# Performance work log

Measured on AMD Instinct MI355X. Metric: run time of the kernel, lower is better.

Reference implementation:

```python
import jax, jax.numpy as jnp
import numpy as np

_SQRT1_2 = 0.7071067811865476

B, S, D, N, NCH = 4, 2048, 1024, 32768, 8


def setup_inputs() -> dict:
    key = jax.random.key(0)
    ks = jax.random.split(key, 6)
    return {
        "x": jax.random.normal(ks[0], (B, S, D), jnp.float32),
        "h": jax.random.normal(ks[1], (B, S, D), jnp.float32),
        "emb": jax.random.normal(ks[2], (N, D), jnp.float32),
        "tau_offset": jax.random.normal(ks[3], (B, S, 1), jnp.float32),
        "w_read": jax.random.normal(ks[4], (N, D), jnp.float32),
        "w_write": jax.random.normal(ks[5], (N, D), jnp.float32),
        "n_chunks": NCH,
    }


def _srw_chunked(x, h, emb_unit, tau_offset, w_read, w_write, n_chunks):
    b, s, d = x.shape
    n = emb_unit.shape[0]
    cs = n // n_chunks
    h_bf = h.astype(jnp.bfloat16)
    x_bf = x.astype(jnp.bfloat16)
    emb_bf = emb_unit.astype(jnp.bfloat16)
    read_bf = w_read.astype(jnp.bfloat16)
    write_bf = w_write.astype(jnp.bfloat16)
    z1 = jnp.zeros((b, s, 1), jnp.float32)

    # ---- pass 1: online score statistics over chunks of N ----
    @jax.checkpoint
    def stats_step(carry, i):
        s_sum, sq_sum, cube_sum, ns_sum, ns_sq = carry
        ec = jax.lax.dynamic_slice_in_dim(emb_bf, i * cs, cs, axis=0)
        sc = (h_bf @ ec.T).astype(jnp.float32)  # [B,S,cs]
        s_sum = s_sum + sc.sum(-1, keepdims=True)
        sq_sum = sq_sum + (sc ** 2).sum(-1, keepdims=True)
        cube_sum = cube_sum + (sc ** 3).sum(-1, keepdims=True)
        pns = sc.mean(axis=(0, 1))  # per-neuron mean score [cs]
        return ((s_sum, sq_sum, cube_sum, ns_sum + pns.sum(), ns_sq + (pns ** 2).sum()), None)

    (s_sum, sq_sum, cube_sum, ns_sum, ns_sq), _ = jax.lax.scan(
        stats_step, (z1, z1, z1, jnp.float32(0.0), jnp.float32(0.0)), jnp.arange(n_chunks))

    s_mean = s_sum / n
    s_std = jnp.sqrt(sq_sum / n - s_mean ** 2) + 1e-08
    tau = s_mean + tau_offset * s_std
    cube_mean = cube_sum / n
    central_third = cube_mean - 3.0 * s_mean * s_std ** 2 - s_mean ** 3
    score_skew = jax.lax.stop_gradient((central_third / (s_std ** 3 + 1e-08)).mean())
    mean_score = ns_sum / n
    var_score = ns_sq / n - mean_score ** 2
    score_lb = var_score / (mean_score ** 2 + var_score + 0.01)

    # ---- pass 2: erf-threshold gate + read/write GEMM accumulate ----
    @jax.checkpoint
    def gate_step(carry, i):
        out, wcost, gmax, act, strong, phib, zsum, z075c, z030c, glg = carry
        s0 = i * cs
        ec = jax.lax.dynamic_slice_in_dim(emb_bf, s0, cs, axis=0)
        rc = jax.lax.dynamic_slice_in_dim(read_bf, s0, cs, axis=0)
        wc = jax.lax.dynamic_slice_in_dim(write_bf, s0, cs, axis=0)
        rc = rc / (jnp.linalg.norm(rc, axis=-1, keepdims=True) + 1e-08)
        wc = wc / (jnp.linalg.norm(wc, axis=-1, keepdims=True) + 1e-08)
        z = ((h_bf @ ec.T).astype(jnp.float32) - tau) / s_std  # [B,S,cs]
        phi = 0.5 * (1.0 + jax.lax.erf(z * _SQRT1_2))
        gate = jnp.where(z > 0, z * phi, 0.0)
        xr = x_bf @ rc.T  # [B,S,cs]
        c_out = ((gate.astype(jnp.bfloat16) * xr) @ wc).astype(jnp.float32)  # [B,S,D]
        g_safe = gate + 1e-08
        new = (
            out + c_out,
            wcost + gate.sum(-1, keepdims=True),
            jnp.maximum(gmax, gate.max(-1, keepdims=True)),
            act + (gate > 0.0).astype(jnp.float32).sum(-1, keepdims=True),
            strong + (gate > 0.5).astype(jnp.float32).sum(-1, keepdims=True),
            phib + ((phi > 0.95) | (phi < 0.05)).astype(jnp.float32).sum(-1, keepdims=True),
            zsum + jnp.where(z > 0, z, 0.0).sum(-1, keepdims=True),
            z075c + ((z > 0) & (z < 0.75)).astype(jnp.float32).sum(-1, keepdims=True),
            z030c + ((z > 0) & (z < 0.3)).astype(jnp.float32).sum(-1, keepdims=True),
            glg + (gate * jnp.log(g_safe)).sum(-1, keepdims=True),
        )
        return (new, None)

    init = (jnp.zeros((b, s, d), jnp.float32), z1, jnp.full((b, s, 1), -1e9, jnp.float32),
            z1, z1, z1, z1, z1, z1, z1)
    (raw_out, wcost, gmax, act, strong, phib, zsum, z075c, z030c, glg), _ = jax.lax.scan(
        gate_step, init, jnp.arange(n_chunks))

    den = jnp.maximum(wcost, 1.0)
    out = (raw_out / den).astype(jnp.bfloat16)
    score_std_out = s_std.mean()
    es_out = wcost.mean()
    active_n_mean = act.mean()
    z_mean_active = zsum / (act + 1e-08)
    active_eps = act + 1e-08
    z_lt_075_frac = jax.lax.stop_gradient((z075c / active_eps).mean())
    z_lt_030_frac = jax.lax.stop_gradient((z030c / active_eps).mean())
    tau_abs_mean = jax.lax.stop_gradient(tau).mean()
    active_per_token_std = jax.lax.stop_gradient(act).std()
    gate_sum_eps = wcost + 1e-08
    entropy_per_token = -glg / gate_sum_eps + jnp.log(gate_sum_eps)
    gate_entropy = jax.lax.stop_gradient(entropy_per_token).mean()
    return (out.astype(jnp.float32), act / n, gmax, score_lb, score_std_out, es_out,
            active_n_mean, strong / n, phib / n, z_mean_active, tau_abs_mean,
            z_lt_075_frac, z_lt_030_frac, score_skew, active_per_token_std, gate_entropy)


def reference(x, h, emb, tau_offset, w_read, w_write, n_chunks):
    emb_unit = emb / (jnp.linalg.norm(emb, axis=-1, keepdims=True) + 1e-08)
    return _srw_chunked(x, h, emb_unit, tau_offset, w_read, w_write, n_chunks)
```

## Files before the change

kernel.cpp:

```cpp
#include <hip/hip_runtime.h>

#define DEV __device__ __forceinline__

typedef __attribute__((ext_vector_type(4))) float f32x4;
typedef __attribute__((ext_vector_type(8))) short s16x8;
typedef __attribute__((ext_vector_type(8))) unsigned short u16x8;

static const int NTOK = 8192;
static const int DD   = 1024;
static const int NNEU = 32768;
static const int NC   = 8192;
static const int NREP = 8;

static const int OUT_ACT    = 8388608;
static const int OUT_GMAX   = 8396800;
static const int OUT_SLB    = 8404992;
static const int OUT_SSTD   = 8404993;
static const int OUT_ES     = 8404994;
static const int OUT_ANM    = 8404995;
static const int OUT_STRONG = 8404996;
static const int OUT_PHIB   = 8413188;
static const int OUT_ZMEAN  = 8421380;
static const int OUT_TAUM   = 8429572;
static const int OUT_Z75    = 8429573;
static const int OUT_Z30    = 8429574;
static const int OUT_SKEW   = 8429575;
static const int OUT_ASTD   = 8429576;
static const int OUT_ENT    = 8429577;

DEV unsigned short f2bf(float f){
  unsigned u = __float_as_uint(f);
  u += 0x7fffu + ((u >> 16) & 1u);
  return (unsigned short)(u >> 16);
}
DEV float bf2f(unsigned short h){ return __uint_as_float(((unsigned)h) << 16); }
DEV float rnd_bf(float f){ return bf2f(f2bf(f)); }

template<int AUX>
DEV void gl_lds16(const void* g, void* l){
  __builtin_amdgcn_global_load_lds(
      (const __attribute__((address_space(1))) unsigned int*)g,
      (__attribute__((address_space(3))) unsigned int*)l, 16, 0, AUX);
}

DEV f32x4 mfma16(s16x8 a, s16x8 b, f32x4 c){
  return __builtin_amdgcn_mfma_f32_16x16x32_bf16(a, b, c, 0, 0, 0);
}

template<int AUX>
DEV void stage4(const unsigned short* __restrict__ G, size_t ld, int k0,
                unsigned short* L, int t){
  #pragma unroll
  for (int i = 0; i < 4; i++){
    int ch = i*256 + t;
    int row = ch >> 3, c = ch & 7;
    int cs = c ^ (row & 7);
    int wb = (i*256 + (t & 192)) * 16;
    gl_lds16<AUX>(G + (size_t)row * ld + k0 + cs*8, (char*)L + wb);
  }
}

DEV void stageS(const unsigned short* __restrict__ S0, size_t ldS,
                unsigned short* L, int t){
  #pragma unroll
  for (int i = 0; i < 8; i++){
    int ch = i*256 + t;
    int row = ch >> 4, c = ch & 15;
    int cs = c ^ (row & 15);
    int wb = (i*256 + (t & 192)) * 16;
    gl_lds16<0>(S0 + (size_t)row * ldS + cs*8, (char*)L + wb);
  }
}

DEV s16x8 frg(const unsigned short* L, int R, int kk, int lq){
  int cc = ((kk >> 3) + lq) ^ (R & 7);
  return *(const s16x8*)((const char*)L + R*128 + cc*16);
}

DEV void waitv_bar(){
  asm volatile("s_waitcnt vmcnt(0)" ::: "memory");
  __builtin_amdgcn_s_barrier();
  __builtin_amdgcn_sched_barrier(0);
}

DEV int2 xcd64(){
  int orig = blockIdx.y * 64 + blockIdx.x;
  int xcd = orig & 7, p = orig >> 3;
  int sqy = p >> 6, off = p & 63;
  int2 r;
  r.x = xcd*8 + (off & 7);
  r.y = sqy*8 + (off >> 3);
  return r;
}


template<int RND, int PNS>
__global__ __launch_bounds__(256) void k_rncast(const float* __restrict__ in,
    unsigned short* __restrict__ o, const float* __restrict__ hs,
    float* __restrict__ ns){
  __shared__ float hsh[1024];
  __shared__ float pr[8];
  int t = threadIdx.x, l = t & 63, wv = t >> 6;
  if (PNS){
    for (int i = t; i < 1024; i += 256) hsh[i] = hs[i];
    __syncthreads();
  }
  int row = blockIdx.x * 4 + wv;
  const float4* rp = (const float4*)(in + (size_t)row * DD);
  float4 v[4];
  float ss = 0.f;
  #pragma unroll
  for (int j = 0; j < 4; j++){
    float4 a = rp[j*64 + l];
    if (RND){ a.x = rnd_bf(a.x); a.y = rnd_bf(a.y); a.z = rnd_bf(a.z); a.w = rnd_bf(a.w); }
    v[j] = a;
    ss += a.x*a.x + a.y*a.y + a.z*a.z + a.w*a.w;
  }
  #pragma unroll
  for (int d = 1; d < 64; d <<= 1) ss += __shfl_xor(ss, d);
  float inv = 1.f / (sqrtf(ss) + 1e-8f);
  float dot = 0.f;
  ushort4* op = (ushort4*)(o + (size_t)row * DD);
  #pragma unroll
  for (int j = 0; j < 4; j++){
    ushort4 r;
    r.x = f2bf(v[j].x * inv); r.y = f2bf(v[j].y * inv);
    r.z = f2bf(v[j].z * inv); r.w = f2bf(v[j].w * inv);
    op[j*64 + l] = r;
    if (PNS){
      int c0 = (j*64 + l)*4;
      dot += hsh[c0]*bf2f(r.x) + hsh[c0+1]*bf2f(r.y)
           + hsh[c0+2]*bf2f(r.z) + hsh[c0+3]*bf2f(r.w);
    }
  }
  if (PNS){
    #pragma unroll
    for (int d = 1; d < 64; d <<= 1) dot += __shfl_xor(dot, d);
    if (l == 0){
      float pns = dot * (1.f / 8192.f);
      pr[wv*2] = pns; pr[wv*2 + 1] = pns*pns;
    }
    __syncthreads();
    if (t == 0){
      atomicAdd(ns + 0, pr[0] + pr[2] + pr[4] + pr[6]);
      atomicAdd(ns + 1, pr[1] + pr[3] + pr[5] + pr[7]);
    }
  }
}

__global__ __launch_bounds__(256) void k_wnorm(const float* __restrict__ w_,
                                               float* __restrict__ inv_w){
  int t = threadIdx.x, l = t & 63, wv = t >> 6;
  int row = blockIdx.x * 4 + wv;
  const float4* wp = (const float4*)(w_ + (size_t)row * DD);
  float sw = 0.f;
  #pragma unroll
  for (int j = 0; j < 4; j++){
    float4 c = wp[j*64 + l];
    float c0 = rnd_bf(c.x), c1 = rnd_bf(c.y), c2 = rnd_bf(c.z), c3 = rnd_bf(c.w);
    sw += c0*c0 + c1*c1 + c2*c2 + c3*c3;
  }
  #pragma unroll
  for (int d = 1; d < 64; d <<= 1) sw += __shfl_xor(sw, d);
  if (l == 0) inv_w[row] = 1.f / (sqrtf(sw) + 1e-8f);
}

__global__ __launch_bounds__(256) void k_cast(const float* __restrict__ in,
                                              unsigned short* __restrict__ o){
  size_t i = (size_t)blockIdx.x * 256 + threadIdx.x;
  float4 v = ((const float4*)in)[i];
  ushort4 r;
  r.x = f2bf(v.x); r.y = f2bf(v.y); r.z = f2bf(v.z); r.w = f2bf(v.w);
  ((ushort4*)o)[i] = r;
}

__global__ __launch_bounds__(256) void k_wcnT(const float* __restrict__ w_,
    const float* __restrict__ invw, unsigned short* __restrict__ o){
  __shared__ unsigned short tile[64][65];
  int t = threadIdx.x;
  int n0b = blockIdx.x * 64, d0 = blockIdx.y * 64;
  #pragma unroll
  for (int i = 0; i < 16; i++){
    int idx = t + i*256;
    int r = idx >> 6, c = idx & 63;
    float v = w_[(size_t)(n0b + r) * DD + d0 + c];
    tile[c][r] = f2bf(rnd_bf(v) * invw[n0b + r]);
  }
  __syncthreads();
  #pragma unroll
  for (int i = 0; i < 16; i++){
    int idx = t + i*256;
    int rd = idx >> 6, cn = idx & 63;
    o[(size_t)(d0 + rd) * NNEU + n0b + cn] = tile[rd][cn];
  }
}

__global__ __launch_bounds__(256) void k_hsum(const unsigned short* __restrict__ hb,
                                              float* __restrict__ hs){
  int t = threadIdx.x; int r0 = blockIdx.x * 128;
  float s[4] = {0.f, 0.f, 0.f, 0.f};
  for (int r = 0; r < 128; r++){
    const unsigned short* row = hb + (size_t)(r0 + r) * DD;
    #pragma unroll
    for (int j = 0; j < 4; j++) s[j] += bf2f(row[j*256 + t]);
  }
  #pragma unroll
  for (int j = 0; j < 4; j++) atomicAdd(hs + j*256 + t, s[j]);
}


template<bool DO_STATS>
__global__ __launch_bounds__(256, 2) void k_score(
    const unsigned short* __restrict__ A, const unsigned short* __restrict__ Bm,
    float* __restrict__ s_sum, float* __restrict__ sq_sum, float* __restrict__ cu_sum,
    unsigned short* __restrict__ Sout, int do_store)
{
  __shared__ unsigned short lds[32768];
  const int t = threadIdx.x, l = t & 63, wv = t >> 6;
  const int wm = wv >> 1, wn = wv & 1;
  const int lq = l >> 4, lr = l & 15;
  int2 rm = xcd64();
  const int bx = rm.x, by = rm.y;
  const unsigned short* Ab = A  + (size_t)by * 128 * DD;
  const unsigned short* Bb = Bm + (size_t)bx * 128 * DD;
  f32x4 acc[4][4];
  #pragma unroll
  for (int m = 0; m < 4; m++)
    #pragma unroll
    for (int n = 0; n < 4; n++) acc[m][n] = (f32x4){0.f, 0.f, 0.f, 0.f};

  stage4<0>(Ab, DD, 0, lds, t);
  stage4<0>(Bb, DD, 0, lds + 8192, t);
  waitv_bar();
  int cur = 0;
  for (int ks = 0; ks < 16; ++ks){
    unsigned short* Lc = lds + cur*16384;
    if (ks + 1 < 16){
      unsigned short* Ln = lds + (cur^1)*16384;
      int k0 = (ks+1)*64;
      stage4<0>(Ab, DD, k0, Ln, t);
      stage4<0>(Bb, DD, k0, Ln + 8192, t);
    }
    #pragma unroll
    for (int kk = 0; kk < 64; kk += 32){
      s16x8 af[4], bf4[4];
      #pragma unroll
      for (int m = 0; m < 4; m++) af[m]  = frg(Lc, wm*64 + m*16 + lr, kk, lq);
      #pragma unroll
      for (int n = 0; n < 4; n++) bf4[n] = frg(Lc + 8192, wn*64 + n*16 + lr, kk, lq);
      #pragma unroll
      for (int m = 0; m < 4; m++)
        #pragma unroll
        for (int n = 0; n < 4; n++)
          acc[m][n] = mfma16(af[m], bf4[n], acc[m][n]);
    }
    waitv_bar();
    cur ^= 1;
  }

  unsigned short* sl = lds;
  #pragma unroll
  for (int m = 0; m < 4; m++)
  #pragma unroll
  for (int n = 0; n < 4; n++)
  #pragma unroll
  for (int r = 0; r < 4; r++){
    int rl = wm*64 + m*16 + lq*4 + r;
    int cl = wn*64 + n*16 + lr;
    sl[rl*136 + cl] = f2bf(acc[m][n][r]);
  }
  __syncthreads();

  int row = t >> 1, half = t & 1;
  const unsigned short* sp = &sl[row*136 + half*64];
  unsigned short* Sdst = Sout + (size_t)(by*128 + row) * NC + bx*128 + half*64;
  float s1 = 0.f, s2 = 0.f, s3 = 0.f;
  #pragma unroll
  for (int j = 0; j < 8; j++){
    u16x8 v = *(const u16x8*)(sp + j*8);
    if (do_store) *(u16x8*)(Sdst + j*8) = v;
    if (DO_STATS){
      #pragma unroll
      for (int e = 0; e < 8; e++){
        float f = bf2f(v[e]);
        s1 += f; float f2 = f*f; s2 += f2; s3 += f2*f;
      }
    }
  }
  if (DO_STATS){
    s1 += __shfl_xor(s1, 1); s2 += __shfl_xor(s2, 1); s3 += __shfl_xor(s3, 1);
    if (half == 0){
      int gr = by*128 + row;
      int rep = (bx & 7) * NTOK;
      atomicAdd(s_sum + rep + gr, s1);
      atomicAdd(sq_sum + rep + gr, s2);
      atomicAdd(cu_sum + rep + gr, s3);
    }
  }
}

__global__ __launch_bounds__(256) void k_tau(const float* __restrict__ s_sum,
    const float* __restrict__ sq_sum, const float* __restrict__ tof,
    float* __restrict__ tau, float* __restrict__ rstd){
  int i = blockIdx.x * 256 + threadIdx.x;
  float ssum = 0.f, sqsum = 0.f;
  #pragma unroll
  for (int k = 0; k < NREP; k++){
    ssum  += s_sum[k*NTOK + i];
    sqsum += sq_sum[k*NTOK + i];
  }
  float mean = ssum * (1.f / 32768.f);
  float var  = sqsum * (1.f / 32768.f) - mean*mean;
  float sstd = sqrtf(fmaxf(var, 0.f)) + 1e-8f;
  tau[i]  = mean + tof[i] * sstd;
  rstd[i] = 1.f / sstd;
}

DEV void gate_epilogue(unsigned short* lds, unsigned short* SP,
    const float* tau, const float* rstd, int bx, int by, int t,
    float* wcostp, float* gmaxp, float* actp, float* strongp, float* phibp,
    float* zsump, float* z075p, float* z030p, float* glgp)
{
  int row = t >> 1, half = t & 1;
  int gr = by*128 + row;
  float tauv = tau[gr], rs = rstd[gr];
  unsigned short* Prow = SP + (size_t)gr * NC + bx*128 + half*64;
  float wsum = 0.f, gmx = 0.f, ac = 0.f, stc = 0.f, pb = 0.f;
  float zs = 0.f, z7 = 0.f, z3 = 0.f, gl = 0.f;
  #pragma unroll
  for (int jj = 0; jj < 8; jj++){
    int g  = half*8 + jj;
    int cs = g ^ (row & 15);
    u16x8 s8 = *(const u16x8*)&lds[row*128 + cs*8];
    u16x8 x8 = *(const u16x8*)&lds[16384 + row*128 + cs*8];
    u16x8 pv;
    #pragma unroll
    for (int e = 0; e < 8; e++){
      float sc = bf2f(s8[e]);
      float xr = bf2f(x8[e]);
      float z = (sc - tauv) * rs;
      float phi = 0.5f * (1.0f + erff(z * 0.70710678118654752440f));
      float gate = (z > 0.f) ? z * phi : 0.f;
      wsum += gate; gmx = fmaxf(gmx, gate);
      if (gate > 0.5f) stc += 1.f;
      if (fabsf(z) > 1.6448536f) pb += 1.f;
      if (z > 0.f){ ac += 1.f; zs += z; if (z < 0.75f) z7 += 1.f; if (z < 0.3f) z3 += 1.f; }
      gl += gate * __logf(gate + 1e-8f);
      pv[e] = f2bf(rnd_bf(gate) * xr);
    }
    *(u16x8*)(Prow + jj*8) = pv;
  }
  wsum += __shfl_xor(wsum, 1); gmx = fmaxf(gmx, __shfl_xor(gmx, 1));
  ac   += __shfl_xor(ac, 1);   stc += __shfl_xor(stc, 1);
  pb   += __shfl_xor(pb, 1);   zs  += __shfl_xor(zs, 1);
  z7   += __shfl_xor(z7, 1);   z3  += __shfl_xor(z3, 1);
  gl   += __shfl_xor(gl, 1);
  if (half == 0){
    int rep = (bx & 7) * NTOK;
    atomicAdd(wcostp + rep + gr, wsum);
    atomicMax((int*)(gmaxp + rep + gr), __float_as_int(gmx));
    atomicAdd(actp + rep + gr, ac);
    atomicAdd(strongp + rep + gr, stc);
    atomicAdd(phibp + rep + gr, pb);
    atomicAdd(zsump + rep + gr, zs);
    atomicAdd(z075p + rep + gr, z7);
    atomicAdd(z030p + rep + gr, z3);
    atomicAdd(glgp + rep + gr, gl);
  }
}


__global__ __launch_bounds__(256, 2) void k_gateS(
    const unsigned short* __restrict__ Xb, const unsigned short* __restrict__ Rb,
    const float* __restrict__ tau, const float* __restrict__ rstd,
    unsigned short* __restrict__ SP, int n0,
    float* __restrict__ wcostp, float* __restrict__ gmaxp, float* __restrict__ actp,
    float* __restrict__ strongp, float* __restrict__ phibp, float* __restrict__ zsump,
    float* __restrict__ z075p, float* __restrict__ z030p, float* __restrict__ glgp)
{
  __shared__ unsigned short lds[32768];
  const int t = threadIdx.x, l = t & 63, wv = t >> 6;
  const int wm = wv >> 1, wn = wv & 1;
  const int lq = l >> 4, lr = l & 15;
  int2 rm = xcd64();
  const int bx = rm.x, by = rm.y;
  const unsigned short* Xp = Xb + (size_t)by * 128 * DD;
  const unsigned short* Rp = Rb + (size_t)(n0 + bx*128) * DD;
  const unsigned short* Stile = SP + (size_t)(by*128) * NC + bx*128;
  f32x4 accX[4][4];
  #pragma unroll
  for (int m = 0; m < 4; m++)
    #pragma unroll
    for (int n = 0; n < 4; n++) accX[m][n] = (f32x4){0.f,0.f,0.f,0.f};

  stage4<0>(Xp, DD, 0, lds, t);
  stage4<0>(Rp, DD, 0, lds + 8192, t);
  waitv_bar();
  int cur = 0;
  for (int ks = 0; ks < 16; ++ks){
    unsigned short* Lc = lds + cur*16384;
    if (ks + 1 < 16){
      unsigned short* Ln = lds + (cur^1)*16384;
      int k0 = (ks+1)*64;
      stage4<0>(Xp, DD, k0, Ln, t);
      stage4<0>(Rp, DD, k0, Ln + 8192, t);
    } else {
      stageS(Stile, NC, lds, t);
    }
    #pragma unroll
    for (int kk = 0; kk < 64; kk += 32){
      s16x8 af[4], bf4[4];
      #pragma unroll
      for (int m = 0; m < 4; m++) af[m]  = frg(Lc, wm*64 + m*16 + lr, kk, lq);
      #pragma unroll
      for (int n = 0; n < 4; n++) bf4[n] = frg(Lc + 8192, wn*64 + n*16 + lr, kk, lq);
      #pragma unroll
      for (int m = 0; m < 4; m++)
        #pragma unroll
        for (int n = 0; n < 4; n++)
          accX[m][n] = mfma16(af[m], bf4[n], accX[m][n]);
    }
    waitv_bar();
    cur ^= 1;
  }
  unsigned short* xrl = lds + 16384;
  #pragma unroll
  for (int m = 0; m < 4; m++)
  #pragma unroll
  for (int n = 0; n < 4; n++)
  #pragma unroll
  for (int r = 0; r < 4; r++){
    int rl = wm*64 + m*16 + lq*4 + r;
    int cl = wn*64 + n*16 + lr;
    int cs = (cl >> 3) ^ (rl & 15);
    xrl[rl*128 + cs*8 + (cl & 7)] = f2bf(accX[m][n][r]);
  }
  __syncthreads();

  gate_epilogue(lds, SP, tau, rstd, bx, by, t,
      wcostp, gmaxp, actp, strongp, phibp, zsump, z075p, z030p, glgp);
}


__global__ __launch_bounds__(256, 2) void k_gate_dual(
    const unsigned short* __restrict__ Hb, const unsigned short* __restrict__ Ec,
    const unsigned short* __restrict__ Xb, const unsigned short* __restrict__ Rc,
    const float* __restrict__ tau, const float* __restrict__ rstd,
    unsigned short* __restrict__ SP,
    float* __restrict__ wcostp, float* __restrict__ gmaxp, float* __restrict__ actp,
    float* __restrict__ strongp, float* __restrict__ phibp, float* __restrict__ zsump,
    float* __restrict__ z075p, float* __restrict__ z030p, float* __restrict__ glgp)
{
  __shared__ unsigned short lds[32768];
  const int t = threadIdx.x, l = t & 63, wv = t >> 6;
  const int wm = wv >> 1, wn = wv & 1;
  const int lq = l >> 4, lr = l & 15;
  int2 rm = xcd64();
  const int bx = rm.x, by = rm.y;
  const unsigned short* Hp = Hb + (size_t)by * 128 * DD;
  const unsigned short* Xp = Xb + (size_t)by * 128 * DD;
  const unsigned short* Ep = Ec + (size_t)(bx*128) * DD;
  const unsigned short* Rp = Rc + (size_t)(bx*128) * DD;
  f32x4 accS[4][4], accX[4][4];
  #pragma unroll
  for (int m = 0; m < 4; m++)
    #pragma unroll
    for (int n = 0; n < 4; n++){
      accS[m][n] = (f32x4){0.f,0.f,0.f,0.f};
      accX[m][n] = (f32x4){0.f,0.f,0.f,0.f};
    }

  for (int k0 = 0; k0 < DD; k0 += 64){
    __syncthreads();
    stage4<0>(Hp, DD, k0, lds +     0, t);
    stage4<0>(Ep, DD, k0, lds +  8192, t);
    stage4<0>(Xp, DD, k0, lds + 16384, t);
    stage4<0>(Rp, DD, k0, lds + 24576, t);
    asm volatile("s_waitcnt vmcnt(0)" ::: "memory");
    __syncthreads();
    #pragma unroll
    for (int kk = 0; kk < 64; kk += 32){
      s16x8 af[4], bf4[4];
      #pragma unroll
      for (int m = 0; m < 4; m++) af[m]  = frg(lds, wm*64 + m*16 + lr, kk, lq);
      #pragma unroll
      for (int n = 0; n < 4; n++) bf4[n] = frg(lds + 8192, wn*64 + n*16 + lr, kk, lq);
      #pragma unroll
      for (int m = 0; m < 4; m++)
        #pragma unroll
        for (int n = 0; n < 4; n++)
          accS[m][n] = mfma16(af[m], bf4[n], accS[m][n]);
      #pragma unroll
      for (int m = 0; m < 4; m++) af[m]  = frg(lds + 16384, wm*64 + m*16 + lr, kk, lq);
      #pragma unroll
      for (int n = 0; n < 4; n++) bf4[n] = frg(lds + 24576, wn*64 + n*16 + lr, kk, lq);
      #pragma unroll
      for (int m = 0; m < 4; m++)
        #pragma unroll
        for (int n = 0; n < 4; n++)
          accX[m][n] = mfma16(af[m], bf4[n], accX[m][n]);
    }
  }
  __syncthreads();
  #pragma unroll
  for (int m = 0; m < 4; m++)
  #pragma unroll
  for (int n = 0; n < 4; n++)
  #pragma unroll
  for (int r = 0; r < 4; r++){
    int rl = wm*64 + m*16 + lq*4 + r;
    int cl = wn*64 + n*16 + lr;
    int cs = (cl >> 3) ^ (rl & 15);
    lds[rl*128 + cs*8 + (cl & 7)]         = f2bf(accS[m][n][r]);
    lds[16384 + rl*128 + cs*8 + (cl & 7)] = f2bf(accX[m][n][r]);
  }
  __syncthreads();

  gate_epilogue(lds, SP, tau, rstd, bx, by, t,
      wcostp, gmaxp, actp, strongp, phibp, zsump, z075p, z030p, glgp);
}

__global__ __launch_bounds__(256) void k_redw(const float* __restrict__ wcostp,
                                              float* __restrict__ wc){
  int i = blockIdx.x * 256 + threadIdx.x;
  float s = 0.f;
  #pragma unroll
  for (int k = 0; k < NREP; k++) s += wcostp[k*NTOK + i];
  wc[i] = s;
}


__global__ __launch_bounds__(256, 2) void k_out_gemm(
    const unsigned short* __restrict__ Pm, const unsigned short* __restrict__ Bt,
    float* __restrict__ outp, const float* __restrict__ wcost, int accum, int fin)
{
  __shared__ unsigned short lds[32768];
  const int t = threadIdx.x, l = t & 63, wv = t >> 6;
  const int wm = wv >> 1, wn = wv & 1;
  const int lq = l >> 4, lr = l & 15;
  const int bx = blockIdx.x, by = blockIdx.y;
  const unsigned short* Ab = Pm + (size_t)by * 128 * NC;
  const unsigned short* Bb = Bt + (size_t)bx * 128 * NNEU;
  f32x4 acc[4][4];
  #pragma unroll
  for (int m = 0; m < 4; m++)
    #pragma unroll
    for (int n = 0; n < 4; n++) acc[m][n] = (f32x4){0.f,0.f,0.f,0.f};

  const int NT = NC / 64;
  stage4<2>(Ab, NC, 0, lds, t);
  stage4<0>(Bb, NNEU, 0, lds + 8192, t);
  waitv_bar();
  int cur = 0;
  for (int ks = 0; ks < NT; ++ks){
    unsigned short* Lc = lds + cur*16384;
    if (ks + 1 < NT){
      unsigned short* Ln = lds + (cur^1)*16384;
      int k0 = (ks+1)*64;
      stage4<2>(Ab, NC, k0, Ln, t);
      stage4<0>(Bb, NNEU, k0, Ln + 8192, t);
    }
    #pragma unroll
    for (int kk = 0; kk < 64; kk += 32){
      s16x8 af[4], bf4[4];
      #pragma unroll
      for (int m = 0; m < 4; m++) af[m]  = frg(Lc, wm*64 + m*16 + lr, kk, lq);
      #pragma unroll
      for (int n = 0; n < 4; n++) bf4[n] = frg(Lc + 8192, wn*64 + n*16 + lr, kk, lq);
      #pragma unroll
      for (int m = 0; m < 4; m++)
        #pragma unroll
        for (int n = 0; n < 4; n++)
          acc[m][n] = mfma16(af[m], bf4[n], acc[m][n]);
    }
    waitv_bar();
    cur ^= 1;
  }
  #pragma unroll
  for (int m = 0; m < 4; m++)
  #pragma unroll
  for (int r = 0; r < 4; r++){
    int gr = by*128 + wm*64 + m*16 + lq*4 + r;
    float den = fin ? fmaxf(wcost[gr], 1.f) : 1.f;
    #pragma unroll
    for (int n = 0; n < 4; n++){
      int dc = bx*128 + wn*64 + n*16 + lr;
      float* o = outp + (size_t)gr * DD + dc;
      float v = acc[m][n][r];
      if (accum) v += *o;
      if (fin)   v = rnd_bf(v / den);
      *o = v;
    }
  }
}


__global__ __launch_bounds__(1024) void k_final(
    const float* __restrict__ s_sum, const float* __restrict__ sq_sum,
    const float* __restrict__ cu_sum, const float* __restrict__ tof,
    const float* __restrict__ wcostp, const float* __restrict__ gmaxp,
    const float* __restrict__ actp, const float* __restrict__ strongp,
    const float* __restrict__ phibp, const float* __restrict__ zsump,
    const float* __restrict__ z075p, const float* __restrict__ z030p,
    const float* __restrict__ glgp, const float* __restrict__ ns,
    float* __restrict__ out)
{
  int tid = threadIdx.x;
  float s0=0,s1=0,s2=0,s3=0,s4=0,s5=0,s6=0,s7=0,s8=0;
  for (int i = tid; i < NTOK; i += 1024){
    float ssum=0, sqsum=0, cusum=0, wc=0, gmax=0, ac=0, stc=0, pb=0, zsv=0, z7=0, z3=0, glv=0;
    #pragma unroll
    for (int k = 0; k < NREP; k++){
      int o = k*NTOK + i;
      ssum += s_sum[o]; sqsum += sq_sum[o]; cusum += cu_sum[o];
      wc += wcostp[o]; gmax = fmaxf(gmax, gmaxp[o]);
      ac += actp[o]; stc += strongp[o]; pb += phibp[o];
      zsv += zsump[o]; z7 += z075p[o]; z3 += z030p[o]; glv += glgp[o];
    }
    float mean = ssum * (1.f / 32768.f);
    float var  = sqsum * (1.f / 32768.f) - mean*mean;
    float sstd = sqrtf(fmaxf(var, 0.f)) + 1e-8f;
    float tauv = mean + tof[i] * sstd;
    out[OUT_ACT + i]    = ac * (1.f / 32768.f);
    out[OUT_GMAX + i]   = gmax;
    out[OUT_STRONG + i] = stc * (1.f / 32768.f);
    out[OUT_PHIB + i]   = pb * (1.f / 32768.f);
    out[OUT_ZMEAN + i]  = zsv / (ac + 1e-8f);
    float c3 = cusum * (1.f / 32768.f) - 3.f*mean*sstd*sstd - mean*mean*mean;
    float skew = c3 / (sstd*sstd*sstd + 1e-8f);
    float gse = wc + 1e-8f;
    float ent = -glv / gse + logf(gse);
    s0 += sstd; s1 += wc; s2 += ac; s3 += ac*ac; s4 += tauv;
    s5 += z7 / (ac + 1e-8f); s6 += z3 / (ac + 1e-8f); s7 += skew; s8 += ent;
  }
  __shared__ float rb[16][9];
  int lane = tid & 63, wid = tid >> 6;
  #pragma unroll
  for (int d = 1; d < 64; d <<= 1){
    s0 += __shfl_xor(s0,d); s1 += __shfl_xor(s1,d); s2 += __shfl_xor(s2,d);
    s3 += __shfl_xor(s3,d); s4 += __shfl_xor(s4,d); s5 += __shfl_xor(s5,d);
    s6 += __shfl_xor(s6,d); s7 += __shfl_xor(s7,d); s8 += __shfl_xor(s8,d);
  }
  if (lane == 0){
    rb[wid][0]=s0; rb[wid][1]=s1; rb[wid][2]=s2; rb[wid][3]=s3; rb[wid][4]=s4;
    rb[wid][5]=s5; rb[wid][6]=s6; rb[wid][7]=s7; rb[wid][8]=s8;
  }
  __syncthreads();
  if (tid == 0){
    float S[9];
    for (int k = 0; k < 9; k++){ float a = 0.f; for (int w2 = 0; w2 < 16; w2++) a += rb[w2][k]; S[k] = a; }
    const float inv = 1.f / 8192.f;
    float act_mean = S[2] * inv;
    out[OUT_SSTD] = S[0] * inv;
    out[OUT_ES]   = S[1] * inv;
    out[OUT_ANM]  = act_mean;
    out[OUT_ASTD] = sqrtf(fmaxf(S[3]*inv - act_mean*act_mean, 0.f));
    out[OUT_TAUM] = S[4] * inv;
    out[OUT_Z75]  = S[5] * inv;
    out[OUT_Z30]  = S[6] * inv;
    out[OUT_SKEW] = S[7] * inv;
    out[OUT_ENT]  = S[8] * inv;
    float ms = ns[0] * (1.f / 32768.f);
    float vs = ns[1] * (1.f / 32768.f) - ms*ms;
    out[OUT_SLB] = vs / (ms*ms + vs + 0.01f);
  }
}


extern "C" void kernel_launch(void* const* d_in, const int* in_sizes, int n_in,
                              void* d_out, int out_size, void* d_ws, size_t ws_size,
                              hipStream_t stream)
{
  (void)in_sizes; (void)n_in; (void)out_size;
  const float* x   = (const float*)d_in[0];
  const float* h   = (const float*)d_in[1];
  const float* emb = (const float*)d_in[2];
  const float* tof = (const float*)d_in[3];
  const float* wr  = (const float*)d_in[4];
  const float* ww  = (const float*)d_in[5];
  float* out = (float*)d_out;
  char* ws = (char*)d_ws;

  size_t off = 0;
  auto get = [&](size_t n){ size_t o = off; off += (n + 255) & ~(size_t)255; return o; };
  unsigned short* rcn_bf = (unsigned short*)(ws + get((size_t)NNEU*DD*2));
  unsigned short* emb_bf = (unsigned short*)(ws + get((size_t)NNEU*DD*2));
  unsigned short* wcnT   = (unsigned short*)(ws + get((size_t)DD*NNEU*2));
  unsigned short* h_bf   = (unsigned short*)(ws + get((size_t)NTOK*DD*2));
  unsigned short* x_bf   = (unsigned short*)(ws + get((size_t)NTOK*DD*2));
  float* inv_w   = (float*)(ws + get(NNEU*4));
  float* tau     = (float*)(ws + get(NTOK*4));
  float* rstd    = (float*)(ws + get(NTOK*4));
  float* wc_comb = (float*)(ws + get(NTOK*4));
  size_t zoff = off;
  float* hsum   = (float*)(ws + get(DD*4));
  float* s_sum  = (float*)(ws + get(NREP*NTOK*4));
  float* sq_sum = (float*)(ws + get(NREP*NTOK*4));
  float* cu_sum = (float*)(ws + get(NREP*NTOK*4));
  float* wcost  = (float*)(ws + get(NREP*NTOK*4));
  float* gmax   = (float*)(ws + get(NREP*NTOK*4));
  float* act    = (float*)(ws + get(NREP*NTOK*4));
  float* strong = (float*)(ws + get(NREP*NTOK*4));
  float* phib   = (float*)(ws + get(NREP*NTOK*4));
  float* zsum   = (float*)(ws + get(NREP*NTOK*4));
  float* z075   = (float*)(ws + get(NREP*NTOK*4));
  float* z030   = (float*)(ws + get(NREP*NTOK*4));
  float* glg    = (float*)(ws + get(NREP*NTOK*4));
  float* ns     = (float*)(ws + get(256));
  size_t zlen = off - zoff;

  const size_t szS = (size_t)NTOK * NC * 2;
  size_t poff = (off + 4095) & ~(size_t)4095;
  size_t avail = ws_size > poff ? ws_size - poff : 0;
  int kst = (int)(avail / szS);
  if (kst > 4) kst = 4;
  if (kst < 1) kst = 1;
  unsigned short* Sb = (unsigned short*)(ws + poff);

  hipMemsetAsync(ws + zoff, 0, zlen, stream);

  dim3 b256(256);
  dim3 gC(64, 64);
  k_cast<<<dim3(NTOK*DD/4/256), b256, 0, stream>>>(h, h_bf);
  k_cast<<<dim3(NTOK*DD/4/256), b256, 0, stream>>>(x, x_bf);
  k_hsum<<<dim3(NTOK/128), b256, 0, stream>>>(h_bf, hsum);
  k_rncast<0,1><<<dim3(NNEU/4), b256, 0, stream>>>(emb, emb_bf, hsum, ns);
  k_rncast<1,0><<<dim3(NNEU/4), b256, 0, stream>>>(wr, rcn_bf, nullptr, nullptr);
  k_wnorm<<<dim3(NNEU/4), b256, 0, stream>>>(ww, inv_w);

  for (int c = 0; c < 4; ++c){
    unsigned short* slot = Sb + (size_t)(c < kst ? c : 0) * NTOK * NC;
    k_score<true><<<gC, b256, 0, stream>>>(h_bf, emb_bf + (size_t)c*NC*DD,
        s_sum, sq_sum, cu_sum, slot, c < kst ? 1 : 0);
  }
  k_tau<<<dim3(NTOK/256), b256, 0, stream>>>(s_sum, sq_sum, tof, tau, rstd);
  k_wcnT<<<dim3(NNEU/64, DD/64), b256, 0, stream>>>(ww, inv_w, wcnT);

  for (int c = 0; c < 4; ++c){
    int slot_i = (c < kst) ? c : (c % kst);
    unsigned short* slot = Sb + (size_t)slot_i * NTOK * NC;
    if (c < kst){
      k_gateS<<<gC, b256, 0, stream>>>(x_bf, rcn_bf, tau, rstd, slot, c*NC,
          wcost, gmax, act, strong, phib, zsum, z075, z030, glg);
    } else {
      k_gate_dual<<<gC, b256, 0, stream>>>(h_bf, emb_bf + (size_t)c*NC*DD,
          x_bf, rcn_bf + (size_t)c*NC*DD, tau, rstd, slot,
          wcost, gmax, act, strong, phib, zsum, z075, z030, glg);
    }
    if (c == 3) k_redw<<<dim3(NTOK/256), b256, 0, stream>>>(wcost, wc_comb);
    k_out_gemm<<<dim3(DD/128, NTOK/128), b256, 0, stream>>>(slot, wcnT + (size_t)c*NC,
        out, wc_comb, c > 0 ? 1 : 0, c == 3 ? 1 : 0);
  }
  k_final<<<dim3(1), dim3(1024), 0, stream>>>(s_sum, sq_sum, cu_sum, tof, wcost, gmax,
      act, strong, phib, zsum, z075, z030, glg, ns, out);
}
```

Before: 3.776 ms.

## Enlarge score GEMM tile to 256x256 with 512 threads, vectorize wcnT and hsum

```diff
diff --git a/kernel.cpp b/kernel.cpp
--- a/kernel.cpp
+++ b/kernel.cpp
@@ -60,6 +60,18 @@
   }
 }
 
+DEV void stage256(const unsigned short* __restrict__ G, size_t ld, int k0,
+                  unsigned short* L, int t){
+  #pragma unroll
+  for (int i = 0; i < 4; i++){
+    int ch = i*512 + t;
+    int row = ch >> 3, c = ch & 7;
+    int cs = c ^ (row & 7);
+    int wb = (i*512 + (t & 448)) * 16;
+    gl_lds16<0>(G + (size_t)row * ld + k0 + cs*8, (char*)L + wb);
+  }
+}
+
 DEV void stageS(const unsigned short* __restrict__ S0, size_t ldS,
                 unsigned short* L, int t){
   #pragma unroll
@@ -90,6 +102,13 @@
   int2 r;
   r.x = xcd*8 + (off & 7);
   r.y = sqy*8 + (off >> 3);
+  return r;
+}
+
+DEV int2 xcd32(){
+  int orig = blockIdx.y * 32 + blockIdx.x;
+  int xcd = orig & 7, p = orig >> 3;
+  int2 r; r.x = xcd*4 + (p & 3); r.y = p >> 2;
   return r;
 }
 
@@ -176,80 +195,88 @@
 
 __global__ __launch_bounds__(256) void k_wcnT(const float* __restrict__ w_,
     const float* __restrict__ invw, unsigned short* __restrict__ o){
-  __shared__ unsigned short tile[64][65];
+  __shared__ unsigned short tile[64][72];
   int t = threadIdx.x;
   int n0b = blockIdx.x * 64, d0 = blockIdx.y * 64;
   #pragma unroll
-  for (int i = 0; i < 16; i++){
-    int idx = t + i*256;
-    int r = idx >> 6, c = idx & 63;
-    float v = w_[(size_t)(n0b + r) * DD + d0 + c];
-    tile[c][r] = f2bf(rnd_bf(v) * invw[n0b + r]);
+  for (int i = 0; i < 4; i++){
+    int ch = i*256 + t;
+    int r = ch >> 4, c4 = ch & 15;
+    float4 v = *(const float4*)&w_[(size_t)(n0b + r) * DD + d0 + c4*4];
+    float iw = invw[n0b + r];
+    tile[c4*4+0][r] = f2bf(rnd_bf(v.x) * iw);
+    tile[c4*4+1][r] = f2bf(rnd_bf(v.y) * iw);
+    tile[c4*4+2][r] = f2bf(rnd_bf(v.z) * iw);
+    tile[c4*4+3][r] = f2bf(rnd_bf(v.w) * iw);
   }
   __syncthreads();
   #pragma unroll
-  for (int i = 0; i < 16; i++){
-    int idx = t + i*256;
-    int rd = idx >> 6, cn = idx & 63;
-    o[(size_t)(d0 + rd) * NNEU + n0b + cn] = tile[rd][cn];
+  for (int i = 0; i < 2; i++){
+    int ch = i*256 + t;
+    int rd = ch >> 3, cn = ch & 7;
+    *(u16x8*)&o[(size_t)(d0 + rd) * NNEU + n0b + cn*8] =
+        *(const u16x8*)&tile[rd][cn*8];
   }
 }
 
 __global__ __launch_bounds__(256) void k_hsum(const unsigned short* __restrict__ hb,
                                               float* __restrict__ hs){
-  int t = threadIdx.x; int r0 = blockIdx.x * 128;
-  float s[4] = {0.f, 0.f, 0.f, 0.f};
-  for (int r = 0; r < 128; r++){
-    const unsigned short* row = hb + (size_t)(r0 + r) * DD;
-    #pragma unroll
-    for (int j = 0; j < 4; j++) s[j] += bf2f(row[j*256 + t]);
-  }
-  #pragma unroll
-  for (int j = 0; j < 4; j++) atomicAdd(hs + j*256 + t, s[j]);
+  int t = threadIdx.x;
+  int colg = (t & 127) * 8;
+  int rh = t >> 7;
+  int r0 = blockIdx.x * 128;
+  float s[8] = {0.f,0.f,0.f,0.f,0.f,0.f,0.f,0.f};
+  for (int r = rh; r < 128; r += 2){
+    u16x8 v = *(const u16x8*)&hb[(size_t)(r0 + r) * DD + colg];
+    #pragma unroll
+    for (int j = 0; j < 8; j++) s[j] += bf2f(v[j]);
+  }
+  #pragma unroll
+  for (int j = 0; j < 8; j++) atomicAdd(hs + colg + j, s[j]);
 }
 
 
 template<bool DO_STATS>
-__global__ __launch_bounds__(256, 2) void k_score(
+__global__ __launch_bounds__(512, 2) void k_score(
     const unsigned short* __restrict__ A, const unsigned short* __restrict__ Bm,
     float* __restrict__ s_sum, float* __restrict__ sq_sum, float* __restrict__ cu_sum,
     unsigned short* __restrict__ Sout, int do_store)
 {
-  __shared__ unsigned short lds[32768];
+  __shared__ unsigned short lds[65536];
   const int t = threadIdx.x, l = t & 63, wv = t >> 6;
-  const int wm = wv >> 1, wn = wv & 1;
+  const int wm = wv >> 2, wn = wv & 3;
   const int lq = l >> 4, lr = l & 15;
-  int2 rm = xcd64();
+  int2 rm = xcd32();
   const int bx = rm.x, by = rm.y;
-  const unsigned short* Ab = A  + (size_t)by * 128 * DD;
-  const unsigned short* Bb = Bm + (size_t)bx * 128 * DD;
-  f32x4 acc[4][4];
-  #pragma unroll
-  for (int m = 0; m < 4; m++)
+  const unsigned short* Ab = A  + (size_t)by * 256 * DD;
+  const unsigned short* Bb = Bm + (size_t)bx * 256 * DD;
+  f32x4 acc[8][4];
+  #pragma unroll
+  for (int m = 0; m < 8; m++)
     #pragma unroll
     for (int n = 0; n < 4; n++) acc[m][n] = (f32x4){0.f, 0.f, 0.f, 0.f};
 
-  stage4<0>(Ab, DD, 0, lds, t);
-  stage4<0>(Bb, DD, 0, lds + 8192, t);
+  stage256(Ab, DD, 0, lds, t);
+  stage256(Bb, DD, 0, lds + 16384, t);
   waitv_bar();
   int cur = 0;
   for (int ks = 0; ks < 16; ++ks){
-    unsigned short* Lc = lds + cur*16384;
+    unsigned short* Lc = lds + cur*32768;
     if (ks + 1 < 16){
-      unsigned short* Ln = lds + (cur^1)*16384;
+      unsigned short* Ln = lds + (cur^1)*32768;
       int k0 = (ks+1)*64;
-      stage4<0>(Ab, DD, k0, Ln, t);
-      stage4<0>(Bb, DD, k0, Ln + 8192, t);
+      stage256(Ab, DD, k0, Ln, t);
+      stage256(Bb, DD, k0, Ln + 16384, t);
     }
     #pragma unroll
     for (int kk = 0; kk < 64; kk += 32){
-      s16x8 af[4], bf4[4];
-      #pragma unroll
-      for (int m = 0; m < 4; m++) af[m]  = frg(Lc, wm*64 + m*16 + lr, kk, lq);
-      #pragma unroll
-      for (int n = 0; n < 4; n++) bf4[n] = frg(Lc + 8192, wn*64 + n*16 + lr, kk, lq);
-      #pragma unroll
-      for (int m = 0; m < 4; m++)
+      s16x8 af[8], bf4[4];
+      #pragma unroll
+      for (int m = 0; m < 8; m++) af[m]  = frg(Lc, wm*128 + m*16 + lr, kk, lq);
+      #pragma unroll
+      for (int n = 0; n < 4; n++) bf4[n] = frg(Lc + 16384, wn*64 + n*16 + lr, kk, lq);
+      #pragma unroll
+      for (int m = 0; m < 8; m++)
         #pragma unroll
         for (int n = 0; n < 4; n++)
           acc[m][n] = mfma16(af[m], bf4[n], acc[m][n]);
@@ -258,26 +285,26 @@
     cur ^= 1;
   }
 
-  unsigned short* sl = lds;
-  #pragma unroll
-  for (int m = 0; m < 4; m++)
+  #pragma unroll
+  for (int m = 0; m < 8; m++)
   #pragma unroll
   for (int n = 0; n < 4; n++)
   #pragma unroll
   for (int r = 0; r < 4; r++){
-    int rl = wm*64 + m*16 + lq*4 + r;
-    int cl = wn*64 + n*16 + lr;
-    sl[rl*136 + cl] = f2bf(acc[m][n][r]);
+    int row = wm*128 + m*16 + lq*4 + r;
+    int cl  = wn*64 + n*16 + lr;
+    int cs  = (cl >> 3) ^ (row & 31);
+    lds[row*256 + cs*8 + (cl & 7)] = f2bf(acc[m][n][r]);
   }
   __syncthreads();
 
   int row = t >> 1, half = t & 1;
-  const unsigned short* sp = &sl[row*136 + half*64];
-  unsigned short* Sdst = Sout + (size_t)(by*128 + row) * NC + bx*128 + half*64;
+  unsigned short* Sdst = Sout + (size_t)(by*256 + row) * NC + bx*256 + half*128;
   float s1 = 0.f, s2 = 0.f, s3 = 0.f;
   #pragma unroll
-  for (int j = 0; j < 8; j++){
-    u16x8 v = *(const u16x8*)(sp + j*8);
+  for (int j = 0; j < 16; j++){
+    int cs = (half*16 + j) ^ (row & 31);
+    u16x8 v = *(const u16x8*)&lds[row*256 + cs*8];
     if (do_store) *(u16x8*)(Sdst + j*8) = v;
     if (DO_STATS){
       #pragma unroll
@@ -290,7 +317,7 @@
   if (DO_STATS){
     s1 += __shfl_xor(s1, 1); s2 += __shfl_xor(s2, 1); s3 += __shfl_xor(s3, 1);
     if (half == 0){
-      int gr = by*128 + row;
+      int gr = by*256 + row;
       int rep = (bx & 7) * NTOK;
       atomicAdd(s_sum + rep + gr, s1);
       atomicAdd(sq_sum + rep + gr, s2);
@@ -719,7 +746,8 @@
 
   hipMemsetAsync(ws + zoff, 0, zlen, stream);
 
-  dim3 b256(256);
+  dim3 b256(256), b512(512);
+  dim3 gC1(32, 32);
   dim3 gC(64, 64);
   k_cast<<<dim3(NTOK*DD/4/256), b256, 0, stream>>>(h, h_bf);
   k_cast<<<dim3(NTOK*DD/4/256), b256, 0, stream>>>(x, x_bf);
@@ -730,7 +758,7 @@
 
   for (int c = 0; c < 4; ++c){
     unsigned short* slot = Sb + (size_t)(c < kst ? c : 0) * NTOK * NC;
-    k_score<true><<<gC, b256, 0, stream>>>(h_bf, emb_bf + (size_t)c*NC*DD,
+    k_score<true><<<gC1, b512, 0, stream>>>(h_bf, emb_bf + (size_t)c*NC*DD,
         s_sum, sq_sum, cu_sum, slot, c < kst ? 1 : 0);
   }
   k_tau<<<dim3(NTOK/256), b256, 0, stream>>>(s_sum, sq_sum, tof, tau, rstd);
```

Result: no change. 3.830 ms (+1.4%).
